# Performance work log

Hardware: AMD Instinct MI355X
Metric: run time of the kernel (lower is better)

Reference implementation:

```python
import jax, jax.numpy as jnp
import numpy as np

B, S, DIM, H = 2, 2048, 512, 8
DEPTH = DIM // H


def setup_inputs() -> dict:
    key = jax.random.key(0)
    ks = jax.random.split(key, 6)
    scale = 1.0 / np.sqrt(DIM)
    X = jax.random.normal(ks[0], (B, S, DIM), dtype=jnp.float32)
    mask = jax.random.randint(ks[1], (B, S), 0, 2).astype(jnp.float32)
    Wq = jax.random.normal(ks[2], (DIM, DIM), dtype=jnp.float32) * scale
    Wk = jax.random.normal(ks[3], (DIM, DIM), dtype=jnp.float32) * scale
    Wv = jax.random.normal(ks[4], (DIM, DIM), dtype=jnp.float32) * scale
    Wo = jax.random.normal(ks[5], (DIM, DIM), dtype=jnp.float32) * scale
    z = jnp.zeros((DIM,), dtype=jnp.float32)
    return {"X": X, "mask": mask, "Wq": Wq, "bq": z, "Wk": Wk, "bk": z,
            "Wv": Wv, "bv": z, "Wo": Wo, "bo": z}


def _split_heads(t):
    # [B, S, DIM] -> [B, H, S, DEPTH]
    return t.reshape(B, S, H, DEPTH).transpose(0, 2, 1, 3)


def reference(X, mask, Wq, bq, Wk, bk, Wv, bv, Wo, bo):
    Q = _split_heads(X @ Wq + bq)
    K = _split_heads(X @ Wk + bk)
    V = _split_heads(X @ Wv + bv)
    # logits: [B, H, Sq, Sk]
    logits = jnp.einsum('bhqd,bhkd->bhqk', Q, K) / jnp.sqrt(jnp.float32(DEPTH))
    logits = logits + mask[:, None, None, :] * (-1e9)
    attn = jax.nn.softmax(logits, axis=-1)
    ctx = jnp.einsum('bhqk,bhkd->bhqd', attn, V)  # [B, H, S, DEPTH]
    concat = ctx.transpose(0, 2, 1, 3).reshape(B, S, DIM)
    out = concat @ Wo + bo
    return (out, attn)
```

## Files before the change

### kernel.cpp

```cpp
#include <hip/hip_runtime.h>
#include <cmath>

#define NB 2
#define SEQ 2048
#define DIM 512
#define NH 8
#define DEPTH 64
#define NT (SEQ / 64)

typedef _Float16 f16_t;
typedef _Float16 f16x8 __attribute__((ext_vector_type(8)));
typedef float f32x4 __attribute__((ext_vector_type(4)));

#define MFMA16(a, b, c) __builtin_amdgcn_mfma_f32_16x16x32_f16((a), (b), (c), 0, 0, 0)

__global__ __launch_bounds__(256) void wprep_kernel(
    const float* __restrict__ Wq, const float* __restrict__ Wk,
    const float* __restrict__ Wv, const float* __restrict__ Wo,
    f16_t* __restrict__ wt, f16_t* __restrict__ wot)
{
    __shared__ float Ws[64][68];
    const int bx = blockIdx.x;
    const int z  = bx >> 6;
    const int kt = (bx >> 3) & 7;
    const int nt = bx & 7;
    const float* W = (z == 0) ? Wq : (z == 1) ? Wk : (z == 2) ? Wv : Wo;
    const int k0 = kt * 64, n0 = nt * 64;
    const int t = threadIdx.x;
    {
        const int r = t >> 2, c0 = (t & 3) * 16;
        #pragma unroll
        for (int j = 0; j < 4; ++j)
            *(f32x4*)&Ws[r][c0 + j*4] =
                *(const f32x4*)&W[(size_t)(k0 + r) * DIM + n0 + c0 + j*4];
    }
    __syncthreads();
    const int n = t >> 2, kc = (t & 3) * 16;
    f16x8 b0, b1;
    #pragma unroll
    for (int j = 0; j < 8; ++j) {
        b0[j] = (f16_t)Ws[kc + j][n];
        b1[j] = (f16_t)Ws[kc + 8 + j][n];
    }
    f16_t* dst = (z < 3) ? (wt + ((size_t)(z * DIM + n0 + n)) * DIM + k0 + kc)
                         : (wot + (size_t)(n0 + n) * DIM + k0 + kc);
    *(f16x8*)dst = b0;
    *(f16x8*)(dst + 8) = b1;
}

__global__ __launch_bounds__(256, 2) void qkv_gemm_kernel(
    const float* __restrict__ X, const f16_t* __restrict__ wt,
    const float* __restrict__ bq, const float* __restrict__ bk,
    const float* __restrict__ bv,
    f16_t* __restrict__ q_h, f16_t* __restrict__ k_h, f16_t* __restrict__ v_t)
{
    const int bx = blockIdx.x;
    const int mb = bx & 31, nb = bx >> 5;
    const int tid = threadIdx.x;
    const int w = tid >> 6, lane = tid & 63, l15 = lane & 15, g4 = lane >> 4;
    const int mBase = mb * 128 + (w >> 1) * 64;
    const int nBase = nb * 128 + (w & 1) * 64;

    f32x4 acc[4][4];
    #pragma unroll
    for (int i = 0; i < 4; ++i)
        #pragma unroll
        for (int j = 0; j < 4; ++j) acc[i][j] = (f32x4){0.f, 0.f, 0.f, 0.f};

    for (int k0 = 0; k0 < DIM; k0 += 64) {
        f16x8 ah[4][2];
        #pragma unroll
        for (int mt = 0; mt < 4; ++mt) {
            const float* xr = X + (size_t)(mBase + mt*16 + l15) * DIM + k0 + g4*8;
            #pragma unroll
            for (int kk = 0; kk < 2; ++kk) {
                f32x4 v0 = *(const f32x4*)(xr + kk*32);
                f32x4 v1 = *(const f32x4*)(xr + kk*32 + 4);
                f16x8 a;
                #pragma unroll
                for (int j = 0; j < 4; ++j) { a[j] = (f16_t)v0[j]; a[j+4] = (f16_t)v1[j]; }
                ah[mt][kk] = a;
            }
        }
        #pragma unroll
        for (int nt = 0; nt < 4; ++nt) {
            const f16_t* wr = wt + (size_t)(nBase + nt*16 + l15) * DIM + k0 + g4*8;
            #pragma unroll
            for (int kk = 0; kk < 2; ++kk) {
                f16x8 bw = *(const f16x8*)(wr + kk*32);
                #pragma unroll
                for (int mt = 0; mt < 4; ++mt)
                    acc[mt][nt] = MFMA16(ah[mt][kk], bw, acc[mt][nt]);
            }
        }
    }

    const int z = nb >> 2;
    const float* bias = (z == 0) ? bq : (z == 1) ? bk : bv;
    #pragma unroll
    for (int mt = 0; mt < 4; ++mt) {
        #pragma unroll
        for (int nt = 0; nt < 4; ++nt) {
            const int n = nBase + nt*16 + l15;
            const int col = n & 511;
            const int h = (n >> 6) & 7, d = n & 63;
            const float bb = bias[col];
            #pragma unroll
            for (int r = 0; r < 4; ++r) {
                const int m = mBase + mt*16 + g4*4 + r;
                const int b = m >> 11, s = m & (SEQ - 1);
                const int bh = b * NH + h;
                const float v = acc[mt][nt][r] + bb;
                if (z == 2) {
                    v_t[((size_t)bh * DEPTH + d) * SEQ + s] = (f16_t)v;
                } else {
                    const size_t o = ((size_t)bh * SEQ + s) * DEPTH + d;
                    if (z == 0) q_h[o] = (f16_t)v;
                    else        k_h[o] = (f16_t)v;
                }
            }
        }
    }
}

__global__ __launch_bounds__(256, 2) void attn_kernel(
    const f16_t* __restrict__ q_h, const f16_t* __restrict__ k_h,
    const f16_t* __restrict__ v_t, const float* __restrict__ mask,
    float* __restrict__ attn, f16_t* __restrict__ ctxf)
{
    __shared__ __align__(16) unsigned char smem[54784];
    f16_t (*Kh)[64][72] = (f16_t(*)[64][72])smem;
    f16_t (*Vt)[64][72] = (f16_t(*)[64][72])(smem + 18432);
    float (*p_all)[68]  = (float(*)[68])(smem + 36864);
    float (*mask_s)[64] = (float(*)[64])(smem + 54272);
    float (*cx)[68]     = (float(*)[68])smem;

    const int tid = threadIdx.x;
    const int w = tid >> 6, lane = tid & 63;
    const int l15 = lane & 15, g4 = lane >> 4;
    const int rr = tid >> 2;
    const int cc = (tid & 3) << 4;

    const int id  = blockIdx.x;
    const int nid = (id & 7) * 64 + (id >> 3);
    const int bh = nid >> 5, qt = nid & 31;
    const int b = bh >> 3, h = bh & 7;

    const size_t kvb = (size_t)bh * SEQ * DEPTH;
    const f16_t* khp = k_h + kvb;
    const f16_t* vtp = v_t + kvb;
    const float* mp  = mask + b * SEQ;
    float* attn_p = attn + (size_t)bh * SEQ * SEQ;

    const int qb = qt * 64;
    const int qw = qb + w * 16;

    f16x8 qf0, qf1;
    {
        const f16_t* qr = q_h + kvb + (size_t)(qw + l15) * DEPTH + g4 * 8;
        qf0 = *(const f16x8*)qr;
        qf1 = *(const f16x8*)(qr + 32);
    }

    float m_r = -INFINITY, l_r = 0.f;

    {
        const f16_t* s0 = khp + (size_t)rr * DEPTH + cc;
        *(uint4*)&Kh[0][rr][cc]     = *(const uint4*)s0;
        *(uint4*)&Kh[0][rr][cc + 8] = *(const uint4*)(s0 + 8);
        if (tid < 64) mask_s[0][tid] = mp[tid];
    }
    __syncthreads();

    int cur = 0;
    for (int kt = 0; kt < NT; ++kt) {
        const bool have = (kt + 1) < NT;
        uint4 nk0, nk1; float nm = 0.f;
        if (have) {
            const f16_t* src = khp + (size_t)((kt+1)*64 + rr) * DEPTH + cc;
            nk0 = *(const uint4*)src;
            nk1 = *(const uint4*)(src + 8);
            if (tid < 64) nm = mp[(kt+1)*64 + tid];
        }

        float sv[4][4];
        #pragma unroll
        for (int nt = 0; nt < 4; ++nt) {
            const f16x8 a0 = *(const f16x8*)&Kh[cur][nt*16 + l15][g4*8];
            const f16x8 a1 = *(const f16x8*)&Kh[cur][nt*16 + l15][32 + g4*8];
            const f32x4 mb = *(const f32x4*)&mask_s[cur][nt*16 + g4*4];
            __builtin_amdgcn_s_setprio(1);
            f32x4 c = {0.f, 0.f, 0.f, 0.f};
            c = MFMA16(a0, qf0, c);
            c = MFMA16(a1, qf1, c);
            __builtin_amdgcn_s_setprio(0);
            #pragma unroll
            for (int r = 0; r < 4; ++r)
                sv[nt][r] = c[r] * 0.125f + mb[r] * (-1e9f);
        }
        float rm = sv[0][0];
        #pragma unroll
        for (int nt = 0; nt < 4; ++nt)
            #pragma unroll
            for (int r = 0; r < 4; ++r) rm = fmaxf(rm, sv[nt][r]);
        rm = fmaxf(rm, __shfl_xor(rm, 16));
        rm = fmaxf(rm, __shfl_xor(rm, 32));
        const float mn = fmaxf(m_r, rm);
        float ts = 0.f;
        #pragma unroll
        for (int nt = 0; nt < 4; ++nt)
            #pragma unroll
            for (int r = 0; r < 4; ++r) ts += __expf(sv[nt][r] - mn);
        ts += __shfl_xor(ts, 16);
        ts += __shfl_xor(ts, 32);
        l_r = l_r * __expf(m_r - mn) + ts;
        m_r = mn;

        if (have) {
            *(uint4*)&Kh[cur ^ 1][rr][cc]     = nk0;
            *(uint4*)&Kh[cur ^ 1][rr][cc + 8] = nk1;
            if (tid < 64) mask_s[cur ^ 1][tid] = nm;
        }
        __syncthreads();
        cur ^= 1;
    }
    const float invl = 1.0f / l_r;

    f32x4 cacc[4];
    #pragma unroll
    for (int nt = 0; nt < 4; ++nt) cacc[nt] = (f32x4){0.f, 0.f, 0.f, 0.f};

    {
        const f16_t* s0 = khp + (size_t)rr * DEPTH + cc;
        *(uint4*)&Kh[0][rr][cc]     = *(const uint4*)s0;
        *(uint4*)&Kh[0][rr][cc + 8] = *(const uint4*)(s0 + 8);
        const f16_t* s1 = vtp + (size_t)rr * SEQ + cc;
        *(uint4*)&Vt[0][rr][cc]     = *(const uint4*)s1;
        *(uint4*)&Vt[0][rr][cc + 8] = *(const uint4*)(s1 + 8);
        if (tid < 64) mask_s[0][tid] = mp[tid];
    }
    __syncthreads();

    cur = 0;
    for (int kt = 0; kt < NT; ++kt) {
        const int kbase = kt * 64;
        const bool have = (kt + 1) < NT;
        uint4 nk0, nk1, nv0, nv1; float nm = 0.f;
        if (have) {
            const f16_t* srck = khp + (size_t)(kbase + 64 + rr) * DEPTH + cc;
            nk0 = *(const uint4*)srck;
            nk1 = *(const uint4*)(srck + 8);
            const f16_t* srcv = vtp + (size_t)rr * SEQ + kbase + 64 + cc;
            nv0 = *(const uint4*)srcv;
            nv1 = *(const uint4*)(srcv + 8);
            if (tid < 64) nm = mp[kbase + 64 + tid];
        }

        #pragma unroll
        for (int nt = 0; nt < 4; ++nt) {
            const f16x8 a0 = *(const f16x8*)&Kh[cur][nt*16 + l15][g4*8];
            const f16x8 a1 = *(const f16x8*)&Kh[cur][nt*16 + l15][32 + g4*8];
            const f32x4 mb = *(const f32x4*)&mask_s[cur][nt*16 + g4*4];
            __builtin_amdgcn_s_setprio(1);
            f32x4 c = {0.f, 0.f, 0.f, 0.f};
            c = MFMA16(a0, qf0, c);
            c = MFMA16(a1, qf1, c);
            __builtin_amdgcn_s_setprio(0);
            f32x4 pv;
            #pragma unroll
            for (int r = 0; r < 4; ++r)
                pv[r] = __expf(c[r] * 0.125f + mb[r] * (-1e9f) - m_r) * invl;
            *(f32x4*)&p_all[w*16 + l15][nt*16 + g4*4] = pv;
        }
        asm volatile("s_waitcnt lgkmcnt(0)" ::: "memory");
        __builtin_amdgcn_sched_barrier(0);

        #pragma unroll
        for (int kk = 0; kk < 2; ++kk) {
            const float* pr = &p_all[w*16 + l15][kk*32 + g4*8];
            const f32x4 p0 = *(const f32x4*)pr;
            const f32x4 p1 = *(const f32x4*)(pr + 4);
            f16x8 pf;
            #pragma unroll
            for (int j = 0; j < 4; ++j) { pf[j] = (f16_t)p0[j]; pf[j+4] = (f16_t)p1[j]; }
            __builtin_amdgcn_s_setprio(1);
            #pragma unroll
            for (int nt = 0; nt < 4; ++nt) {
                const f16x8 vf = *(const f16x8*)&Vt[cur][nt*16 + l15][kk*32 + g4*8];
                cacc[nt] = MFMA16(vf, pf, cacc[nt]);
            }
            __builtin_amdgcn_s_setprio(0);
        }

        #pragma unroll
        for (int j = 0; j < 4; ++j) {
            const int qloc = j*4 + g4;
            const f32x4 pv = *(const f32x4*)&p_all[w*16 + qloc][l15*4];
            __builtin_nontemporal_store(
                pv, (f32x4*)(attn_p + (size_t)(qw + qloc) * SEQ + kbase + l15*4));
        }

        if (have) {
            *(uint4*)&Kh[cur ^ 1][rr][cc]     = nk0;
            *(uint4*)&Kh[cur ^ 1][rr][cc + 8] = nk1;
            *(uint4*)&Vt[cur ^ 1][rr][cc]     = nv0;
            *(uint4*)&Vt[cur ^ 1][rr][cc + 8] = nv1;
            if (tid < 64) mask_s[cur ^ 1][tid] = nm;
        }
        __syncthreads();
        cur ^= 1;
    }

    #pragma unroll
    for (int nt = 0; nt < 4; ++nt)
        #pragma unroll
        for (int r = 0; r < 4; ++r)
            cx[nt*16 + g4*4 + r][w*16 + l15] = cacc[nt][r];
    __syncthreads();
    {
        const int q = tid >> 2, dc = (tid & 3) << 4;
        f16x8 o0, o1;
        #pragma unroll
        for (int j = 0; j < 8; ++j) {
            o0[j] = (f16_t)cx[dc + j][q];
            o1[j] = (f16_t)cx[dc + 8 + j][q];
        }
        f16_t* dst = ctxf + ((size_t)(b * SEQ) + qb + q) * DIM + h * 64 + dc;
        *(f16x8*)dst = o0;
        *(f16x8*)(dst + 8) = o1;
    }
}

__global__ __launch_bounds__(256, 2) void out_gemm_kernel(
    const f16_t* __restrict__ ctxf, const f16_t* __restrict__ wot,
    const float* __restrict__ bo, float* __restrict__ out)
{
    const int bx = blockIdx.x;
    const int mb = bx & 63, nb = bx >> 6;
    const int tid = threadIdx.x;
    const int w = tid >> 6, lane = tid & 63, l15 = lane & 15, g4 = lane >> 4;
    const int mBase = mb * 64 + (w >> 1) * 32;
    const int nBase = nb * 128 + (w & 1) * 64;

    f32x4 acc[2][4];
    #pragma unroll
    for (int i = 0; i < 2; ++i)
        #pragma unroll
        for (int j = 0; j < 4; ++j) acc[i][j] = (f32x4){0.f, 0.f, 0.f, 0.f};

    for (int k0 = 0; k0 < DIM; k0 += 64) {
        f16x8 ah[2][2];
        #pragma unroll
        for (int mt = 0; mt < 2; ++mt) {
            const f16_t* ar = ctxf + (size_t)(mBase + mt*16 + l15) * DIM + k0 + g4*8;
            ah[mt][0] = *(const f16x8*)ar;
            ah[mt][1] = *(const f16x8*)(ar + 32);
        }
        #pragma unroll
        for (int nt = 0; nt < 4; ++nt) {
            const f16_t* wr = wot + (size_t)(nBase + nt*16 + l15) * DIM + k0 + g4*8;
            #pragma unroll
            for (int kk = 0; kk < 2; ++kk) {
                f16x8 bw = *(const f16x8*)(wr + kk*32);
                #pragma unroll
                for (int mt = 0; mt < 2; ++mt)
                    acc[mt][nt] = MFMA16(ah[mt][kk], bw, acc[mt][nt]);
            }
        }
    }
    #pragma unroll
    for (int mt = 0; mt < 2; ++mt) {
        #pragma unroll
        for (int nt = 0; nt < 4; ++nt) {
            const int n = nBase + nt*16 + l15;
            const float bn = bo[n];
            #pragma unroll
            for (int r = 0; r < 4; ++r) {
                const int m = mBase + mt*16 + g4*4 + r;
                out[(size_t)m * DIM + n] = acc[mt][nt][r] + bn;
            }
        }
    }
}

extern "C" void kernel_launch(void* const* d_in, const int* in_sizes, int n_in,
                              void* d_out, int out_size, void* d_ws, size_t ws_size,
                              hipStream_t stream)
{
    const float* X    = (const float*)d_in[0];
    const float* mask = (const float*)d_in[1];
    const float* Wq   = (const float*)d_in[2];
    const float* bq   = (const float*)d_in[3];
    const float* Wk   = (const float*)d_in[4];
    const float* bk   = (const float*)d_in[5];
    const float* Wv   = (const float*)d_in[6];
    const float* bv   = (const float*)d_in[7];
    const float* Wo   = (const float*)d_in[8];
    const float* bo   = (const float*)d_in[9];

    float* out  = (float*)d_out;
    float* attn = out + (size_t)NB * SEQ * DIM;

    const size_t N = (size_t)NB * NH * SEQ * DEPTH;
    f16_t* q_h  = (f16_t*)d_ws;
    f16_t* k_h  = q_h + N;
    f16_t* v_t  = k_h + N;
    f16_t* wt   = v_t + N;
    f16_t* wot  = wt + (size_t)3 * DIM * DIM;
    f16_t* ctxf = wot + (size_t)DIM * DIM;

    wprep_kernel<<<256, 256, 0, stream>>>(Wq, Wk, Wv, Wo, wt, wot);

    qkv_gemm_kernel<<<384, 256, 0, stream>>>(X, wt, bq, bk, bv, q_h, k_h, v_t);

    attn_kernel<<<512, 256, 0, stream>>>(q_h, k_h, v_t, mask, attn, ctxf);

    out_gemm_kernel<<<256, 256, 0, stream>>>(ctxf, wot, bo, out);
}
```

Baseline: 170.9 us.

## Precast X to fp16, read mask from global, store attn directly, retile out GEMM

Adds an fp16 conversion of X to the prep kernel so the QKV GEMM loads half-width operands and does no per-tile conversion. The attention kernel drops the LDS mask buffer and reads mask values straight from global memory into registers. It writes attention probabilities from registers instead of re-reading them from LDS. Barriers become a waitcnt plus s_barrier with a scheduling barrier. The output GEMM tile is halved to launch twice as many blocks. In exchange the attn stores become less coalesced (16-byte pieces per row), and the final ctx transpose now uses only a wave-local wait before reading LDS written by other waves, which is a possible race.

Result: slower. 185.7 us (+8.7%).

```diff
diff --git a/kernel.cpp b/kernel.cpp
--- a/kernel.cpp
+++ b/kernel.cpp
@@ -14,13 +14,29 @@
 
 #define MFMA16(a, b, c) __builtin_amdgcn_mfma_f32_16x16x32_f16((a), (b), (c), 0, 0, 0)
 
-__global__ __launch_bounds__(256) void wprep_kernel(
+#define LDS_BARRIER() do { \
+    asm volatile("s_waitcnt lgkmcnt(0)\n\ts_barrier" ::: "memory"); \
+    __builtin_amdgcn_sched_barrier(0); \
+} while (0)
+
+__global__ __launch_bounds__(256) void prep_kernel(
+    const float* __restrict__ X,
     const float* __restrict__ Wq, const float* __restrict__ Wk,
     const float* __restrict__ Wv, const float* __restrict__ Wo,
-    f16_t* __restrict__ wt, f16_t* __restrict__ wot)
+    f16_t* __restrict__ wt, f16_t* __restrict__ wot, f16_t* __restrict__ xh)
 {
+    const int bx = blockIdx.x;
+    if (bx >= 256) {
+        const size_t i = ((size_t)(bx - 256) * 256 + threadIdx.x) * 8;
+        const f32x4 a = *(const f32x4*)(X + i);
+        const f32x4 b = *(const f32x4*)(X + i + 4);
+        f16x8 o;
+        #pragma unroll
+        for (int j = 0; j < 4; ++j) { o[j] = (f16_t)a[j]; o[j+4] = (f16_t)b[j]; }
+        *(f16x8*)(xh + i) = o;
+        return;
+    }
     __shared__ float Ws[64][68];
-    const int bx = blockIdx.x;
     const int z  = bx >> 6;
     const int kt = (bx >> 3) & 7;
     const int nt = bx & 7;
@@ -49,7 +65,7 @@
 }
 
 __global__ __launch_bounds__(256, 2) void qkv_gemm_kernel(
-    const float* __restrict__ X, const f16_t* __restrict__ wt,
+    const f16_t* __restrict__ xh, const f16_t* __restrict__ wt,
     const float* __restrict__ bq, const float* __restrict__ bk,
     const float* __restrict__ bv,
     f16_t* __restrict__ q_h, f16_t* __restrict__ k_h, f16_t* __restrict__ v_t)
@@ -71,16 +87,9 @@
         f16x8 ah[4][2];
         #pragma unroll
         for (int mt = 0; mt < 4; ++mt) {
-            const float* xr = X + (size_t)(mBase + mt*16 + l15) * DIM + k0 + g4*8;
-            #pragma unroll
-            for (int kk = 0; kk < 2; ++kk) {
-                f32x4 v0 = *(const f32x4*)(xr + kk*32);
-                f32x4 v1 = *(const f32x4*)(xr + kk*32 + 4);
-                f16x8 a;
-                #pragma unroll
-                for (int j = 0; j < 4; ++j) { a[j] = (f16_t)v0[j]; a[j+4] = (f16_t)v1[j]; }
-                ah[mt][kk] = a;
-            }
+            const f16_t* xr = xh + (size_t)(mBase + mt*16 + l15) * DIM + k0 + g4*8;
+            ah[mt][0] = *(const f16x8*)xr;
+            ah[mt][1] = *(const f16x8*)(xr + 32);
         }
         #pragma unroll
         for (int nt = 0; nt < 4; ++nt) {
@@ -128,18 +137,15 @@
     const f16_t* __restrict__ v_t, const float* __restrict__ mask,
     float* __restrict__ attn, f16_t* __restrict__ ctxf)
 {
-    __shared__ __align__(16) unsigned char smem[54784];
-    f16_t (*Kh)[64][72] = (f16_t(*)[64][72])smem;
-    f16_t (*Vt)[64][72] = (f16_t(*)[64][72])(smem + 18432);
-    float (*p_all)[68]  = (float(*)[68])(smem + 36864);
-    float (*mask_s)[64] = (float(*)[64])(smem + 54272);
-    float (*cx)[68]     = (float(*)[68])smem;
+    __shared__ __align__(16) f16_t Kh[2][64][72];
+    __shared__ __align__(16) f16_t Vt[2][64][72];
+    __shared__ __align__(16) float p_all[64][68];
+    float (*cx)[68] = (float(*)[68])&Kh[0][0][0];
 
     const int tid = threadIdx.x;
     const int w = tid >> 6, lane = tid & 63;
     const int l15 = lane & 15, g4 = lane >> 4;
-    const int rr = tid >> 2;
-    const int cc = (tid & 3) << 4;
+    const int rr = tid >> 2, cc = (tid & 3) << 4;
 
     const int id  = blockIdx.x;
     const int nid = (id & 7) * 64 + (id >> 3);
@@ -168,27 +174,30 @@
         const f16_t* s0 = khp + (size_t)rr * DEPTH + cc;
         *(uint4*)&Kh[0][rr][cc]     = *(const uint4*)s0;
         *(uint4*)&Kh[0][rr][cc + 8] = *(const uint4*)(s0 + 8);
-        if (tid < 64) mask_s[0][tid] = mp[tid];
-    }
-    __syncthreads();
+    }
+    LDS_BARRIER();
 
     int cur = 0;
     for (int kt = 0; kt < NT; ++kt) {
+        const int kbase = kt * 64;
+        f32x4 mb[4];
+        #pragma unroll
+        for (int nt = 0; nt < 4; ++nt)
+            mb[nt] = *(const f32x4*)(mp + kbase + nt*16 + g4*4);
+
         const bool have = (kt + 1) < NT;
-        uint4 nk0, nk1; float nm = 0.f;
+        uint4 nk0, nk1;
         if (have) {
             const f16_t* src = khp + (size_t)((kt+1)*64 + rr) * DEPTH + cc;
             nk0 = *(const uint4*)src;
             nk1 = *(const uint4*)(src + 8);
-            if (tid < 64) nm = mp[(kt+1)*64 + tid];
-        }
-
-        float sv[4][4];
+        }
+
+        float s[4][4];
         #pragma unroll
         for (int nt = 0; nt < 4; ++nt) {
             const f16x8 a0 = *(const f16x8*)&Kh[cur][nt*16 + l15][g4*8];
             const f16x8 a1 = *(const f16x8*)&Kh[cur][nt*16 + l15][32 + g4*8];
-            const f32x4 mb = *(const f32x4*)&mask_s[cur][nt*16 + g4*4];
             __builtin_amdgcn_s_setprio(1);
             f32x4 c = {0.f, 0.f, 0.f, 0.f};
             c = MFMA16(a0, qf0, c);
@@ -196,13 +205,13 @@
             __builtin_amdgcn_s_setprio(0);
             #pragma unroll
             for (int r = 0; r < 4; ++r)
-                sv[nt][r] = c[r] * 0.125f + mb[r] * (-1e9f);
-        }
-        float rm = sv[0][0];
+                s[nt][r] = c[r] * 0.125f + mb[nt][r] * (-1e9f);
+        }
+        float rm = s[0][0];
         #pragma unroll
         for (int nt = 0; nt < 4; ++nt)
             #pragma unroll
-            for (int r = 0; r < 4; ++r) rm = fmaxf(rm, sv[nt][r]);
+            for (int r = 0; r < 4; ++r) rm = fmaxf(rm, s[nt][r]);
         rm = fmaxf(rm, __shfl_xor(rm, 16));
         rm = fmaxf(rm, __shfl_xor(rm, 32));
         const float mn = fmaxf(m_r, rm);
@@ -210,7 +219,7 @@
         #pragma unroll
         for (int nt = 0; nt < 4; ++nt)
             #pragma unroll
-            for (int r = 0; r < 4; ++r) ts += __expf(sv[nt][r] - mn);
+            for (int r = 0; r < 4; ++r) ts += __expf(s[nt][r] - mn);
         ts += __shfl_xor(ts, 16);
         ts += __shfl_xor(ts, 32);
         l_r = l_r * __expf(m_r - mn) + ts;
@@ -219,9 +228,8 @@
         if (have) {
             *(uint4*)&Kh[cur ^ 1][rr][cc]     = nk0;
             *(uint4*)&Kh[cur ^ 1][rr][cc + 8] = nk1;
-            if (tid < 64) mask_s[cur ^ 1][tid] = nm;
-        }
-        __syncthreads();
+        }
+        LDS_BARRIER();
         cur ^= 1;
     }
     const float invl = 1.0f / l_r;
@@ -237,15 +245,19 @@
         const f16_t* s1 = vtp + (size_t)rr * SEQ + cc;
         *(uint4*)&Vt[0][rr][cc]     = *(const uint4*)s1;
         *(uint4*)&Vt[0][rr][cc + 8] = *(const uint4*)(s1 + 8);
-        if (tid < 64) mask_s[0][tid] = mp[tid];
-    }
-    __syncthreads();
+    }
+    LDS_BARRIER();
 
     cur = 0;
     for (int kt = 0; kt < NT; ++kt) {
         const int kbase = kt * 64;
+        f32x4 mb[4];
+        #pragma unroll
+        for (int nt = 0; nt < 4; ++nt)
+            mb[nt] = *(const f32x4*)(mp + kbase + nt*16 + g4*4);
+
         const bool have = (kt + 1) < NT;
-        uint4 nk0, nk1, nv0, nv1; float nm = 0.f;
+        uint4 nk0, nk1, nv0, nv1;
         if (have) {
             const f16_t* srck = khp + (size_t)(kbase + 64 + rr) * DEPTH + cc;
             nk0 = *(const uint4*)srck;
@@ -253,14 +265,12 @@
             const f16_t* srcv = vtp + (size_t)rr * SEQ + kbase + 64 + cc;
             nv0 = *(const uint4*)srcv;
             nv1 = *(const uint4*)(srcv + 8);
-            if (tid < 64) nm = mp[kbase + 64 + tid];
         }
 
         #pragma unroll
         for (int nt = 0; nt < 4; ++nt) {
             const f16x8 a0 = *(const f16x8*)&Kh[cur][nt*16 + l15][g4*8];
             const f16x8 a1 = *(const f16x8*)&Kh[cur][nt*16 + l15][32 + g4*8];
-            const f32x4 mb = *(const f32x4*)&mask_s[cur][nt*16 + g4*4];
             __builtin_amdgcn_s_setprio(1);
             f32x4 c = {0.f, 0.f, 0.f, 0.f};
             c = MFMA16(a0, qf0, c);
@@ -269,7 +279,9 @@
             f32x4 pv;
             #pragma unroll
             for (int r = 0; r < 4; ++r)
-                pv[r] = __expf(c[r] * 0.125f + mb[r] * (-1e9f) - m_r) * invl;
+                pv[r] = __expf(c[r] * 0.125f + mb[nt][r] * (-1e9f) - m_r) * invl;
+            __builtin_nontemporal_store(
+                pv, (f32x4*)(attn_p + (size_t)(qw + l15) * SEQ + kbase + nt*16 + g4*4));
             *(f32x4*)&p_all[w*16 + l15][nt*16 + g4*4] = pv;
         }
         asm volatile("s_waitcnt lgkmcnt(0)" ::: "memory");
@@ -292,22 +304,13 @@
             __builtin_amdgcn_s_setprio(0);
         }
 
-        #pragma unroll
-        for (int j = 0; j < 4; ++j) {
-            const int qloc = j*4 + g4;
-            const f32x4 pv = *(const f32x4*)&p_all[w*16 + qloc][l15*4];
-            __builtin_nontemporal_store(
-                pv, (f32x4*)(attn_p + (size_t)(qw + qloc) * SEQ + kbase + l15*4));
-        }
-
         if (have) {
             *(uint4*)&Kh[cur ^ 1][rr][cc]     = nk0;
             *(uint4*)&Kh[cur ^ 1][rr][cc + 8] = nk1;
             *(uint4*)&Vt[cur ^ 1][rr][cc]     = nv0;
             *(uint4*)&Vt[cur ^ 1][rr][cc + 8] = nv1;
-            if (tid < 64) mask_s[cur ^ 1][tid] = nm;
-        }
-        __syncthreads();
+        }
+        LDS_BARRIER();
         cur ^= 1;
     }
 
@@ -316,7 +319,8 @@
         #pragma unroll
         for (int r = 0; r < 4; ++r)
             cx[nt*16 + g4*4 + r][w*16 + l15] = cacc[nt][r];
-    __syncthreads();
+    asm volatile("s_waitcnt lgkmcnt(0)" ::: "memory");
+    __builtin_amdgcn_sched_barrier(0);
     {
         const int q = tid >> 2, dc = (tid & 3) << 4;
         f16x8 o0, o1;
@@ -340,13 +344,13 @@
     const int tid = threadIdx.x;
     const int w = tid >> 6, lane = tid & 63, l15 = lane & 15, g4 = lane >> 4;
     const int mBase = mb * 64 + (w >> 1) * 32;
-    const int nBase = nb * 128 + (w & 1) * 64;
-
-    f32x4 acc[2][4];
+    const int nBase = nb * 64 + (w & 1) * 32;
+
+    f32x4 acc[2][2];
     #pragma unroll
     for (int i = 0; i < 2; ++i)
         #pragma unroll
-        for (int j = 0; j < 4; ++j) acc[i][j] = (f32x4){0.f, 0.f, 0.f, 0.f};
+        for (int j = 0; j < 2; ++j) acc[i][j] = (f32x4){0.f, 0.f, 0.f, 0.f};
 
     for (int k0 = 0; k0 < DIM; k0 += 64) {
         f16x8 ah[2][2];
@@ -357,7 +361,7 @@
             ah[mt][1] = *(const f16x8*)(ar + 32);
         }
         #pragma unroll
-        for (int nt = 0; nt < 4; ++nt) {
+        for (int nt = 0; nt < 2; ++nt) {
             const f16_t* wr = wot + (size_t)(nBase + nt*16 + l15) * DIM + k0 + g4*8;
             #pragma unroll
             for (int kk = 0; kk < 2; ++kk) {
@@ -371,7 +375,7 @@
     #pragma unroll
     for (int mt = 0; mt < 2; ++mt) {
         #pragma unroll
-        for (int nt = 0; nt < 4; ++nt) {
+        for (int nt = 0; nt < 2; ++nt) {
             const int n = nBase + nt*16 + l15;
             const float bn = bo[n];
             #pragma unroll
@@ -408,12 +412,13 @@
     f16_t* wt   = v_t + N;
     f16_t* wot  = wt + (size_t)3 * DIM * DIM;
     f16_t* ctxf = wot + (size_t)DIM * DIM;
-
-    wprep_kernel<<<256, 256, 0, stream>>>(Wq, Wk, Wv, Wo, wt, wot);
-
-    qkv_gemm_kernel<<<384, 256, 0, stream>>>(X, wt, bq, bk, bv, q_h, k_h, v_t);
+    f16_t* xh   = ctxf + N;
+
+    prep_kernel<<<1280, 256, 0, stream>>>(X, Wq, Wk, Wv, Wo, wt, wot, xh);
+
+    qkv_gemm_kernel<<<384, 256, 0, stream>>>(xh, wt, bq, bk, bv, q_h, k_h, v_t);
 
     attn_kernel<<<512, 256, 0, stream>>>(q_h, k_h, v_t, mask, attn, ctxf);
 
-    out_gemm_kernel<<<256, 256, 0, stream>>>(ctxf, wot, bo, out);
+    out_gemm_kernel<<<512, 256, 0, stream>>>(ctxf, wot, bo, out);
 }
```
